# Kernel optimization log

Measured on AMD Instinct MI355X. Metric: run time of the kernel, lower is better.

Reference implementation:

```python
import jax, jax.numpy as jnp
import numpy as np

B, LQ, LK, D = 8, 2048, 2048, 128

def setup_inputs() -> dict:
    key = jax.random.key(0)
    k1, k2, k3, k4 = jax.random.split(key, 4)
    return {
        "query": jax.random.normal(k1, (B, LQ, D), dtype=jnp.float32),
        "key": jax.random.normal(k2, (B, LK, D), dtype=jnp.float32),
        "value": jax.random.normal(k3, (B, LK, D), dtype=jnp.float32),
        "scale_factor": jax.random.normal(k4, (B, LQ, LK), dtype=jnp.float32),
    }

def reference(query, key, value, scale_factor):
    # qk: [B, LQ, LK]
    qk = jnp.einsum("bqd,bkd->bqk", query, key)
    probs = jax.nn.softmax(qk * scale_factor, axis=-1)
    # dropout_p = 0.0 -> identity
    return jnp.einsum("bqk,bkd->bqd", probs, value)
```

## Files before the change

kernel.cpp:

```cpp
#include <hip/hip_runtime.h>
#include <hip/hip_bf16.h>


typedef float          f32x4 __attribute__((ext_vector_type(4)));
typedef short          s16x8 __attribute__((ext_vector_type(8)));
typedef unsigned int   u32x4 __attribute__((ext_vector_type(4)));
typedef unsigned short u16x4 __attribute__((ext_vector_type(4)));

#define LOG2E 1.4426950408889634f

__device__ __forceinline__ float fast_exp2(float x) {
#if __has_builtin(__builtin_amdgcn_exp2f)
    return __builtin_amdgcn_exp2f(x);
#else
    return exp2f(x);
#endif
}

__device__ __forceinline__ unsigned short f2bf(float x) {
    return __builtin_bit_cast(unsigned short, __float2bfloat16(x));
}
__device__ __forceinline__ float bf2f(unsigned short u) {
    return __bfloat162float(__builtin_bit_cast(__hip_bfloat16, u));
}

__global__ void conv_split(const float* __restrict__ src,
                           unsigned short* __restrict__ hi,
                           unsigned short* __restrict__ lo, int n4) {
    int i = blockIdx.x * blockDim.x + threadIdx.x;
    if (i >= n4) return;
    const float4 v = ((const float4*)src)[i];
    float f[4] = {v.x, v.y, v.z, v.w};
    u16x4 h, l;
#pragma unroll
    for (int j = 0; j < 4; ++j) {
        unsigned short hb = f2bf(f[j]);
        h[j] = hb;
        l[j] = f2bf(f[j] - bf2f(hb));
    }
    ((u16x4*)hi)[i] = h;
    ((u16x4*)lo)[i] = l;
}

__global__ void transpose_v(const float* __restrict__ v,
                            unsigned short* __restrict__ vt) {
    __shared__ unsigned short tile[64 * 132];
    const int b   = blockIdx.x & 7;
    const int k0  = (blockIdx.x >> 3) * 64;
    const int tid = threadIdx.x;
#pragma unroll
    for (int p = 0; p < 8; ++p) {
        int idx  = p * 256 + tid;
        int k    = idx >> 5;
        int dblk = idx & 31;
        float4 val = ((const float4*)v)[((b * 2048 + k0 + k) * 128 + dblk * 4) >> 2];
        u16x4 t4;
        t4[0] = f2bf(val.x); t4[1] = f2bf(val.y);
        t4[2] = f2bf(val.z); t4[3] = f2bf(val.w);
        *(u16x4*)&tile[k * 132 + dblk * 4] = t4;
    }
    __syncthreads();
#pragma unroll
    for (int p = 0; p < 4; ++p) {
        int idx = p * 256 + tid;
        int d   = idx >> 3;
        int k8  = idx & 7;
        u16x4 a, c;
#pragma unroll
        for (int j = 0; j < 4; ++j) a[j] = tile[(k8 * 8 + j) * 132 + d];
#pragma unroll
        for (int j = 0; j < 4; ++j) c[j] = tile[(k8 * 8 + 4 + j) * 132 + d];
        unsigned short* outp = vt + (b * 128 + d) * 2048 + k0 + k8 * 8;
        *(u16x4*)outp       = a;
        *(u16x4*)(outp + 4) = c;
    }
}

#define KHS 136
#define VTS 72
#define PS  72

__global__ __launch_bounds__(256, 2)
void flash_fwd(const unsigned short* __restrict__ qh_g,
               const unsigned short* __restrict__ ql_g,
               const unsigned short* __restrict__ kh_g,
               const unsigned short* __restrict__ kl_g,
               const unsigned short* __restrict__ vt_g,
               const float* __restrict__ scale_g,
               float* __restrict__ opart,
               float* __restrict__ mpart,
               float* __restrict__ lpart) {
    __shared__ unsigned short lds_kh[64 * KHS];
    __shared__ unsigned short lds_kl[64 * KHS];
    __shared__ unsigned short lds_vt[128 * VTS];
    __shared__ unsigned short lds_p[4][16 * PS];

    const int tid  = threadIdx.x;
    const int wave = tid >> 6;
    const int lane = tid & 63;
    const int c    = lane & 15;
    const int g    = lane >> 4;

    const int bid   = blockIdx.x;
    const int b     = bid & 7;
    const int qt    = (bid >> 3) & 31;
    const int ks    = bid >> 8;
    const int q0    = qt * 64;
    const int kbase = ks * 1024;

    s16x8 qh[4], ql[4];
    {
        const int qrow = b * 2048 + q0 + wave * 16 + c;
#pragma unroll
        for (int kstep = 0; kstep < 4; ++kstep) {
            int idx = qrow * 16 + kstep * 4 + g;
            qh[kstep] = __builtin_bit_cast(s16x8, ((const u32x4*)qh_g)[idx]);
            ql[kstep] = __builtin_bit_cast(s16x8, ((const u32x4*)ql_g)[idx]);
        }
    }

    f32x4 oacc[8];
#pragma unroll
    for (int t = 0; t < 8; ++t) oacc[t] = (f32x4){0.f, 0.f, 0.f, 0.f};
    float m2[4], ln[4];
#pragma unroll
    for (int r = 0; r < 4; ++r) { m2[r] = -INFINITY; ln[r] = 0.f; }

    for (int kc = 0; kc < 16; ++kc) {
        const int k0 = kbase + kc * 64;

        __syncthreads();
        {
            u32x4 tk[4], tl[4], tv[4];
            const int row = tid >> 4, c8 = tid & 15;
            const int dv  = tid >> 3, k8 = tid & 7;
#pragma unroll
            for (int p = 0; p < 4; ++p) {
                int gidx = (b * 2048 + k0 + p * 16 + row) * 16 + c8;
                tk[p] = ((const u32x4*)kh_g)[gidx];
                tl[p] = ((const u32x4*)kl_g)[gidx];
                int vidx = (b * 128 + p * 32 + dv) * 256 + (k0 >> 3) + k8;
                tv[p] = ((const u32x4*)vt_g)[vidx];
            }
#pragma unroll
            for (int p = 0; p < 4; ++p) {
                *(u32x4*)&lds_kh[(p * 16 + row) * KHS + c8 * 8] = tk[p];
                *(u32x4*)&lds_kl[(p * 16 + row) * KHS + c8 * 8] = tl[p];
                *(u32x4*)&lds_vt[(p * 32 + dv) * VTS + k8 * 8]  = tv[p];
            }
        }
        __syncthreads();

        float sc[4][4];
        {
            const int qrow = b * 2048 + q0 + wave * 16 + g * 4;
#pragma unroll
            for (int r = 0; r < 4; ++r)
#pragma unroll
                for (int t = 0; t < 4; ++t)
                    sc[t][r] = scale_g[(qrow + r) * 2048 + k0 + t * 16 + c] * LOG2E;
        }

        f32x4 s[4];
#pragma unroll
        for (int t = 0; t < 4; ++t) s[t] = (f32x4){0.f, 0.f, 0.f, 0.f};
#pragma unroll
        for (int kstep = 0; kstep < 4; ++kstep) {
#pragma unroll
            for (int t = 0; t < 4; ++t) {
                int off = (t * 16 + c) * KHS + kstep * 32 + g * 8;
                s16x8 bh = *(const s16x8*)&lds_kh[off];
                s16x8 bl = *(const s16x8*)&lds_kl[off];
                s[t] = __builtin_amdgcn_mfma_f32_16x16x32_bf16(qh[kstep], bh, s[t], 0, 0, 0);
                s[t] = __builtin_amdgcn_mfma_f32_16x16x32_bf16(ql[kstep], bh, s[t], 0, 0, 0);
                s[t] = __builtin_amdgcn_mfma_f32_16x16x32_bf16(qh[kstep], bl, s[t], 0, 0, 0);
            }
        }

        float lt[4][4], mx[4];
#pragma unroll
        for (int r = 0; r < 4; ++r) {
            lt[0][r] = s[0][r] * sc[0][r];
            lt[1][r] = s[1][r] * sc[1][r];
            lt[2][r] = s[2][r] * sc[2][r];
            lt[3][r] = s[3][r] * sc[3][r];
            mx[r] = fmaxf(fmaxf(lt[0][r], lt[1][r]), fmaxf(lt[2][r], lt[3][r]));
        }
#pragma unroll
        for (int mask = 1; mask < 16; mask <<= 1)
#pragma unroll
            for (int r = 0; r < 4; ++r)
                mx[r] = fmaxf(mx[r], __shfl_xor(mx[r], mask));
        float al[4], rs[4];
#pragma unroll
        for (int r = 0; r < 4; ++r) {
            float mn = fmaxf(m2[r], mx[r]);
            al[r] = fast_exp2(m2[r] - mn);
            m2[r] = mn;
            rs[r] = 0.f;
        }
#pragma unroll
        for (int t = 0; t < 4; ++t)
#pragma unroll
            for (int r = 0; r < 4; ++r) {
                float p = fast_exp2(lt[t][r] - m2[r]);
                rs[r] += p;
                lds_p[wave][(g * 4 + r) * PS + t * 16 + c] = f2bf(p);
            }
#pragma unroll
        for (int mask = 1; mask < 16; mask <<= 1)
#pragma unroll
            for (int r = 0; r < 4; ++r)
                rs[r] += __shfl_xor(rs[r], mask);
#pragma unroll
        for (int r = 0; r < 4; ++r) ln[r] = ln[r] * al[r] + rs[r];
#pragma unroll
        for (int t = 0; t < 8; ++t)
#pragma unroll
            for (int r = 0; r < 4; ++r) oacc[t][r] *= al[r];

#pragma unroll
        for (int k2 = 0; k2 < 2; ++k2) {
            s16x8 af = *(const s16x8*)&lds_p[wave][c * PS + k2 * 32 + g * 8];
#pragma unroll
            for (int t2 = 0; t2 < 8; ++t2) {
                s16x8 bv = *(const s16x8*)&lds_vt[(t2 * 16 + c) * VTS + k2 * 32 + g * 8];
                oacc[t2] = __builtin_amdgcn_mfma_f32_16x16x32_bf16(af, bv, oacc[t2], 0, 0, 0);
            }
        }
    }

    {
        const int rowb = (ks * 8 + b) * 2048 + q0 + wave * 16;
#pragma unroll
        for (int t2 = 0; t2 < 8; ++t2)
#pragma unroll
            for (int r = 0; r < 4; ++r)
                opart[(rowb + g * 4 + r) * 128 + t2 * 16 + c] = oacc[t2][r];
        if (c == 0) {
#pragma unroll
            for (int r = 0; r < 4; ++r) {
                mpart[rowb + g * 4 + r] = m2[r];
                lpart[rowb + g * 4 + r] = ln[r];
            }
        }
    }
}

__global__ void merge_halves(const float* __restrict__ opart,
                             const float* __restrict__ mpart,
                             const float* __restrict__ lpart,
                             float* __restrict__ out) {
    const int row = blockIdx.x;
    const int d   = threadIdx.x;
    const float m0 = mpart[row],  m1 = mpart[16384 + row];
    const float l0 = lpart[row],  l1 = lpart[16384 + row];
    const float M  = fmaxf(m0, m1);
    const float a0 = fast_exp2(m0 - M);
    const float a1 = fast_exp2(m1 - M);
    const float inv = 1.f / (a0 * l0 + a1 * l1);
    const int i = row * 128 + d;
    out[i] = (a0 * opart[i] + a1 * opart[16384 * 128 + i]) * inv;
}

extern "C" void kernel_launch(void* const* d_in, const int* in_sizes, int n_in,
                              void* d_out, int out_size, void* d_ws, size_t ws_size,
                              hipStream_t stream) {
    const float* q  = (const float*)d_in[0];
    const float* k  = (const float*)d_in[1];
    const float* v  = (const float*)d_in[2];
    const float* sc = (const float*)d_in[3];
    float* out = (float*)d_out;

    char* ws = (char*)d_ws;
    const size_t MB = 1024 * 1024;
    unsigned short* qh = (unsigned short*)(ws);
    unsigned short* ql = (unsigned short*)(ws + 4 * MB);
    unsigned short* kh = (unsigned short*)(ws + 8 * MB);
    unsigned short* kl = (unsigned short*)(ws + 12 * MB);
    unsigned short* vt = (unsigned short*)(ws + 16 * MB);
    float* opart = (float*)(ws + 20 * MB);
    float* mpart = (float*)(ws + 36 * MB);
    float* lpart = (float*)(ws + 36 * MB + 128 * 1024);

    conv_split<<<2048, 256, 0, stream>>>(q, qh, ql, 524288);
    conv_split<<<2048, 256, 0, stream>>>(k, kh, kl, 524288);
    transpose_v<<<256, 256, 0, stream>>>(v, vt);
    flash_fwd<<<512, 256, 0, stream>>>(qh, ql, kh, kl, vt, sc, opart, mpart, lpart);
    merge_halves<<<16384, 128, 0, stream>>>(opart, mpart, lpart, out);
}
```

Baseline: 258.7 us.

## Prefetch next K/V tile and scale block into registers during compute

Loads the next chunk's K-high/K-low/V-transposed tiles and scale_factor values into registers while the current chunk is being computed, then stores them to LDS at the top of the next iteration. This software-pipelines global memory latency behind the MFMA and softmax work instead of stalling on loads right before each use. It costs roughly 64 extra VGPRs (48 for tiles, 16 for scales), which may lower occupancy or cause spills.

```diff
diff --git a/kernel.cpp b/kernel.cpp
--- a/kernel.cpp
+++ b/kernel.cpp
@@ -108,6 +108,9 @@
     const int q0    = qt * 64;
     const int kbase = ks * 1024;
 
+    const int srow = tid >> 4, sc8 = tid & 15;
+    const int sdv  = tid >> 3, sk8 = tid & 7;
+
     s16x8 qh[4], ql[4];
     {
         const int qrow = b * 2048 + q0 + wave * 16 + c;
@@ -126,39 +129,61 @@
 #pragma unroll
     for (int r = 0; r < 4; ++r) { m2[r] = -INFINITY; ln[r] = 0.f; }
 
+    u32x4 pk[4], pl[4], pv[4];
+    float scn[4][4];
+    const int scb = (b * 2048 + q0 + wave * 16 + g * 4) * 2048 + c;
+
+    {
+        const int k0 = kbase;
+#pragma unroll
+        for (int p = 0; p < 4; ++p) {
+            int gidx = (b * 2048 + k0 + p * 16 + srow) * 16 + sc8;
+            pk[p] = ((const u32x4*)kh_g)[gidx];
+            pl[p] = ((const u32x4*)kl_g)[gidx];
+            int vidx = (b * 128 + p * 32 + sdv) * 256 + (k0 >> 3) + sk8;
+            pv[p] = ((const u32x4*)vt_g)[vidx];
+        }
+#pragma unroll
+        for (int t = 0; t < 4; ++t)
+#pragma unroll
+            for (int r = 0; r < 4; ++r)
+                scn[t][r] = scale_g[scb + r * 2048 + k0 + t * 16];
+    }
+
     for (int kc = 0; kc < 16; ++kc) {
         const int k0 = kbase + kc * 64;
 
         __syncthreads();
-        {
-            u32x4 tk[4], tl[4], tv[4];
-            const int row = tid >> 4, c8 = tid & 15;
-            const int dv  = tid >> 3, k8 = tid & 7;
+#pragma unroll
+        for (int p = 0; p < 4; ++p) {
+            *(u32x4*)&lds_kh[(p * 16 + srow) * KHS + sc8 * 8] = pk[p];
+            *(u32x4*)&lds_kl[(p * 16 + srow) * KHS + sc8 * 8] = pl[p];
+            *(u32x4*)&lds_vt[(p * 32 + sdv) * VTS + sk8 * 8]  = pv[p];
+        }
+        __syncthreads();
+
+        float sc[4][4];
+#pragma unroll
+        for (int t = 0; t < 4; ++t)
+#pragma unroll
+            for (int r = 0; r < 4; ++r)
+                sc[t][r] = scn[t][r] * LOG2E;
+
+        if (kc < 15) {
+            const int kn = k0 + 64;
 #pragma unroll
             for (int p = 0; p < 4; ++p) {
-                int gidx = (b * 2048 + k0 + p * 16 + row) * 16 + c8;
-                tk[p] = ((const u32x4*)kh_g)[gidx];
-                tl[p] = ((const u32x4*)kl_g)[gidx];
-                int vidx = (b * 128 + p * 32 + dv) * 256 + (k0 >> 3) + k8;
-                tv[p] = ((const u32x4*)vt_g)[vidx];
-            }
-#pragma unroll
-            for (int p = 0; p < 4; ++p) {
-                *(u32x4*)&lds_kh[(p * 16 + row) * KHS + c8 * 8] = tk[p];
-                *(u32x4*)&lds_kl[(p * 16 + row) * KHS + c8 * 8] = tl[p];
-                *(u32x4*)&lds_vt[(p * 32 + dv) * VTS + k8 * 8]  = tv[p];
-            }
-        }
-        __syncthreads();
-
-        float sc[4][4];
-        {
-            const int qrow = b * 2048 + q0 + wave * 16 + g * 4;
-#pragma unroll
-            for (int r = 0; r < 4; ++r)
-#pragma unroll
-                for (int t = 0; t < 4; ++t)
-                    sc[t][r] = scale_g[(qrow + r) * 2048 + k0 + t * 16 + c] * LOG2E;
+                int gidx = (b * 2048 + kn + p * 16 + srow) * 16 + sc8;
+                pk[p] = ((const u32x4*)kh_g)[gidx];
+                pl[p] = ((const u32x4*)kl_g)[gidx];
+                int vidx = (b * 128 + p * 32 + sdv) * 256 + (kn >> 3) + sk8;
+                pv[p] = ((const u32x4*)vt_g)[vidx];
+            }
+#pragma unroll
+            for (int t = 0; t < 4; ++t)
+#pragma unroll
+                for (int r = 0; r < 4; ++r)
+                    scn[t][r] = scale_g[scb + r * 2048 + kn + t * 16];
         }
 
         f32x4 s[4];
```

Result: faster. 253.6 us (-2.0%).
